# Optimization experiments

Measured on AMD Instinct MI355X. Metric: run time of the kernel, lower is better.

Reference implementation:

```python
import jax, jax.numpy as jnp
import numpy as np

B, T, D, H, E = 4, 2048, 1024, 4096, 8


def setup_inputs() -> dict:
    key = jax.random.key(0)
    ks = jax.random.split(key, 7)
    x = jax.random.normal(ks[0], (B, T, D), dtype=jnp.float32)
    # Gate: Linear(D, E)
    Wg = jax.random.normal(ks[1], (D, E), dtype=jnp.float32) / np.sqrt(D)
    bg = jax.random.normal(ks[2], (E,), dtype=jnp.float32) * 0.01
    # Experts: E x [Linear(D,H), ReLU, Linear(H,D)] (dropout inactive at eval)
    W1 = jax.random.normal(ks[3], (E, D, H), dtype=jnp.float32) / np.sqrt(D)
    b1 = jax.random.normal(ks[4], (E, H), dtype=jnp.float32) * 0.01
    W2 = jax.random.normal(ks[5], (E, H, D), dtype=jnp.float32) / np.sqrt(H)
    b2 = jax.random.normal(ks[6], (E, D), dtype=jnp.float32) * 0.01
    return {"x": x, "Wg": Wg, "bg": bg, "W1": W1, "b1": b1, "W2": W2, "b2": b2}


def reference(x, Wg, bg, W1, b1, W2, b2):
    # Gate + hard top-1 routing
    gate_scores = x @ Wg + bg                      # [B,T,E]
    top1 = jnp.argmax(gate_scores, axis=-1)        # [B,T]
    onehot = jax.nn.one_hot(top1, Wg.shape[-1], dtype=x.dtype)  # [B,T,E]
    # Dense: every expert MLP over all tokens (matches original's masked
    # formulation: x*mask == x on selected tokens, output re-masked).
    h = jax.nn.relu(jnp.einsum('btd,edh->beth', x, W1) + b1[None, :, None, :])
    y = jnp.einsum('beth,ehd->betd', h, W2) + b2[None, :, None, :]
    # Masked combine: keep only the token's chosen expert output
    out = jnp.einsum('betd,bte->btd', y, onehot)
    return out
```

## Files before the change

### kernel.cpp

```cpp
#include <hip/hip_runtime.h>
#include <hip/hip_bf16.h>
#include <stdint.h>

#define NTOK 8192
#define DDIM 1024
#define HDIM 4096
#define NEXP 8
#define MAXWL 72

typedef __attribute__((ext_vector_type(4))) float f32x4;
typedef __attribute__((ext_vector_type(8))) short s16x8;
typedef __attribute__((ext_vector_type(8))) unsigned short u16x8;

__device__ __forceinline__ unsigned short f2bf(float f) {
  union { float f; unsigned int u; } v; v.f = f;
  unsigned int u = v.u;
  u += 0x7FFFu + ((u >> 16) & 1u);
  return (unsigned short)(u >> 16);
}

typedef __attribute__((address_space(3))) unsigned char lds_u8;
typedef const __attribute__((address_space(1))) unsigned char glb_u8;

__device__ __forceinline__ void load_lds16(const void* g, void* l) {
  __builtin_amdgcn_global_load_lds((glb_u8*)g, (lds_u8*)l, 16, 0, 0);
}

__global__ __launch_bounds__(256) void gate_kernel(
    const float* __restrict__ x, const float* __restrict__ Wg,
    const float* __restrict__ bg, int* __restrict__ counts,
    int* __restrict__ lists) {
  const int lane = threadIdx.x & 63;
  const int tok = blockIdx.x * 4 + (threadIdx.x >> 6);
  const float* xr = x + (size_t)tok * DDIM;
  double acc[NEXP];
#pragma unroll
  for (int e = 0; e < NEXP; ++e) acc[e] = 0.0;
#pragma unroll 4
  for (int it = 0; it < DDIM / 64; ++it) {
    const int d = it * 64 + lane;
    const float xv = xr[d];
    const f32x4 w0 = *(const f32x4*)(Wg + (size_t)d * NEXP);
    const f32x4 w1 = *(const f32x4*)(Wg + (size_t)d * NEXP + 4);
#pragma unroll
    for (int j = 0; j < 4; ++j) {
      acc[j]     += (double)xv * (double)w0[j];
      acc[4 + j] += (double)xv * (double)w1[j];
    }
  }
#pragma unroll
  for (int e = 0; e < NEXP; ++e) {
    double v = acc[e];
#pragma unroll
    for (int off = 32; off > 0; off >>= 1) v += __shfl_xor(v, off, 64);
    acc[e] = v;
  }
  if (lane == 0) {
    int best = 0;
    double bv = acc[0] + (double)bg[0];
#pragma unroll
    for (int e = 1; e < NEXP; ++e) {
      const double v = acc[e] + (double)bg[e];
      if (v > bv) { bv = v; best = e; }
    }
    const int pos = atomicAdd(&counts[best], 1);
    lists[best * NTOK + pos] = tok;
  }
}

__global__ void offs_kernel(const int* __restrict__ counts, int* __restrict__ offs,
                            int* __restrict__ wl) {
  int s = 0;
#pragma unroll
  for (int e = 0; e < NEXP; ++e) { offs[e] = s; s += counts[e]; }
  offs[NEXP] = s;
  int n = 0;
  for (int e = 0; e < NEXP; ++e) {
    const int nb = (counts[e] + 127) >> 7;
    for (int b = 0; b < nb; ++b) wl[n++] = (e << 20) | b;
  }
  offs[NEXP + 1] = n;
}

__global__ __launch_bounds__(256) void gather_conv_kernel(
    const float* __restrict__ x, const int* __restrict__ offs,
    const int* __restrict__ lists, int* __restrict__ stok,
    unsigned short* __restrict__ xbs) {
  const int p = blockIdx.x * 4 + (threadIdx.x >> 6);
  const int lane = threadIdx.x & 63;
  int e = 0;
#pragma unroll
  for (int k = 1; k < NEXP; ++k) e += (p >= offs[k]) ? 1 : 0;
  const int tok = lists[e * NTOK + (p - offs[e])];
  if (lane == 0) stok[p] = tok;
  const float* src = x + (size_t)tok * DDIM + lane * 16;
  unsigned short* dst = xbs + (size_t)p * DDIM + lane * 16;
#pragma unroll
  for (int q = 0; q < 2; ++q) {
    const f32x4 a = *(const f32x4*)(src + q * 8);
    const f32x4 b = *(const f32x4*)(src + q * 8 + 4);
    u16x8 o;
#pragma unroll
    for (int j = 0; j < 4; ++j) { o[j] = f2bf(a[j]); o[4 + j] = f2bf(b[j]); }
    *(u16x8*)(dst + q * 8) = o;
  }
}

__global__ __launch_bounds__(256) void transpose_conv_kernel(
    const float* __restrict__ in, unsigned short* __restrict__ out,
    int R, int C) {
  __shared__ unsigned short T[64][66];
  const int e = blockIdx.z;
  const float* ine = in + (size_t)e * R * C;
  unsigned short* oute = out + (size_t)e * C * R;
  const int c0 = blockIdx.x * 64, r0 = blockIdx.y * 64;
  const int t = threadIdx.x;
  const int tr = t >> 4, tc4 = (t & 15) * 4;
#pragma unroll
  for (int p = 0; p < 4; ++p) {
    const int r = tr + p * 16;
    const f32x4 v = *(const f32x4*)(ine + (size_t)(r0 + r) * C + c0 + tc4);
#pragma unroll
    for (int j = 0; j < 4; ++j) T[r][tc4 + j] = f2bf(v[j]);
  }
  __syncthreads();
#pragma unroll
  for (int p = 0; p < 4; ++p) {
    const int c = tr + p * 16;
    ushort4 o;
    o.x = T[tc4 + 0][c]; o.y = T[tc4 + 1][c];
    o.z = T[tc4 + 2][c]; o.w = T[tc4 + 3][c];
    *(ushort4*)(oute + (size_t)(c0 + c) * R + r0 + tc4) = o;
  }
}

template <int K, int N, bool FUSE1>
__global__ __launch_bounds__(256, 2) void ffn_kernel(
    const unsigned short* __restrict__ A, const unsigned short* __restrict__ Bt,
    const float* __restrict__ bias, const int* __restrict__ counts,
    const int* __restrict__ offs, const int* __restrict__ wl,
    const int* __restrict__ stok, unsigned short* __restrict__ outb,
    float* __restrict__ outf) {
  constexpr int BM = 128, BN = 128;
  constexpr int MF = 4, NF = 4;
  constexpr int NT = K / 64;
  static_assert((NT & 1) == 0 && NT >= 4, "");

  if ((int)blockIdx.y >= offs[NEXP + 1]) return;
  const int wle = wl[blockIdx.y];
  const int e = wle >> 20;
  const int bx = wle & 0xFFFFF;
  const int cnt = counts[e];
  const int row0 = offs[e] + bx * BM;
  const int col0 = blockIdx.x * BN;

  __shared__ __align__(16) unsigned short As0[BM][64];
  __shared__ __align__(16) unsigned short Bs0[BN][64];
  __shared__ __align__(16) unsigned short As1[BM][64];
  __shared__ __align__(16) unsigned short Bs1[BN][64];

  const int tid = threadIdx.x;
  const int lane = tid & 63;
  const int w = tid >> 6;
  const int wm = w >> 1;
  const int wn = w & 1;
  const int fr = lane & 15;
  const int fj = lane >> 4;

  const int swz = ((tid & 7) ^ ((tid >> 3) & 7)) * 8;
  const int rb = tid >> 3;
  const unsigned short* srcA[4];
#pragma unroll
  for (int i = 0; i < 4; ++i) {
    int gr = row0 + i * 32 + rb;
    if (gr > NTOK - 1) gr = NTOK - 1;
    srcA[i] = A + (size_t)gr * K + swz;
  }
  const unsigned short* Bte = Bt + (size_t)e * N * K;
  const unsigned short* srcB[4];
#pragma unroll
  for (int i = 0; i < 4; ++i)
    srcB[i] = Bte + (size_t)(col0 + i * 32 + rb) * K + swz;

  f32x4 acc[MF][NF];
#pragma unroll
  for (int m = 0; m < MF; ++m)
#pragma unroll
    for (int n = 0; n < NF; ++n) acc[m][n] = f32x4{0.f, 0.f, 0.f, 0.f};

  auto stage = [&](unsigned short* dA, unsigned short* dB, int k0) {
#pragma unroll
    for (int i = 0; i < 4; ++i)
      load_lds16(srcA[i] + k0, dA + i * 32 * 64 + tid * 8);
#pragma unroll
    for (int i = 0; i < 4; ++i)
      load_lds16(srcB[i] + k0, dB + i * 32 * 64 + tid * 8);
  };

  auto phase = [&](const unsigned short* pA, const unsigned short* pB,
                   unsigned short* nA, unsigned short* nB, int knext,
                   bool do_stage) {
    asm volatile("s_waitcnt vmcnt(0)" ::: "memory");
    __builtin_amdgcn_s_barrier();
    s16x8 af[2][MF], bf[2][NF];
#pragma unroll
    for (int kk = 0; kk < 2; ++kk) {
      const int js = (((kk << 2) + fj) ^ (fr & 7)) << 3;
#pragma unroll
      for (int m = 0; m < MF; ++m)
        af[kk][m] = *(const s16x8*)(pA + (wm * 64 + m * 16 + fr) * 64 + js);
#pragma unroll
      for (int n = 0; n < NF; ++n)
        bf[kk][n] = *(const s16x8*)(pB + (wn * 64 + n * 16 + fr) * 64 + js);
    }
    if (do_stage) stage(nA, nB, knext);
    __builtin_amdgcn_s_setprio(1);
#pragma unroll
    for (int kk = 0; kk < 2; ++kk)
#pragma unroll
      for (int m = 0; m < MF; ++m)
#pragma unroll
        for (int n = 0; n < NF; ++n)
          acc[m][n] = __builtin_amdgcn_mfma_f32_16x16x32_bf16(
              af[kk][m], bf[kk][n], acc[m][n], 0, 0, 0);
    __builtin_amdgcn_s_setprio(0);
  };

  unsigned short* A0 = &As0[0][0];
  unsigned short* B0 = &Bs0[0][0];
  unsigned short* A1 = &As1[0][0];
  unsigned short* B1 = &Bs1[0][0];

  stage(A0, B0, 0);
#pragma unroll 1
  for (int t = 0; t + 2 < NT; t += 2) {
    phase(A0, B0, A1, B1, (t + 1) * 64, true);
    phase(A1, B1, A0, B0, (t + 2) * 64, true);
  }
  phase(A0, B0, A1, B1, (NT - 1) * 64, true);
  phase(A1, B1, A0, B0, 0, false);

#pragma unroll
  for (int n = 0; n < NF; ++n) {
    const int col = col0 + wn * 64 + n * 16 + fr;
    const float bv = bias[e * N + col];
#pragma unroll
    for (int m = 0; m < MF; ++m) {
#pragma unroll
      for (int j = 0; j < 4; ++j) {
        const int rl = wm * 64 + m * 16 + fj * 4 + j;
        if (bx * BM + rl < cnt) {
          if constexpr (FUSE1) {
            outb[(size_t)(row0 + rl) * N + col] = f2bf(fmaxf(acc[m][n][j] + bv, 0.f));
          } else {
            outf[(size_t)stok[row0 + rl] * N + col] = acc[m][n][j] + bv;
          }
        }
      }
    }
  }
}

extern "C" void kernel_launch(void* const* d_in, const int* in_sizes, int n_in,
                              void* d_out, int out_size, void* d_ws, size_t ws_size,
                              hipStream_t stream) {
  (void)in_sizes; (void)n_in; (void)out_size;
  const float* x  = (const float*)d_in[0];
  const float* Wg = (const float*)d_in[1];
  const float* bg = (const float*)d_in[2];
  const float* W1 = (const float*)d_in[3];
  const float* b1 = (const float*)d_in[4];
  const float* W2 = (const float*)d_in[5];
  const float* b2 = (const float*)d_in[6];
  float* out = (float*)d_out;

  char* ws = (char*)d_ws;
  const size_t OFF_CNT = 0;
  const size_t OFF_OFF = 128;
  const size_t OFF_WL  = 256;
  const size_t OFF_LST = 1024;
  const size_t OFF_STK = OFF_LST + (size_t)NEXP * NTOK * 4;
  const size_t OFF_XBS = OFF_STK + (size_t)NTOK * 4;
  const size_t OFF_HS  = OFF_XBS + (size_t)NTOK * DDIM * 2;
  const size_t OFF_WT  = OFF_HS + (size_t)NTOK * HDIM * 2;
  const size_t NEED    = OFF_WT + (size_t)NEXP * DDIM * HDIM * 2;
  if (ws_size < NEED) return;

  int* counts = (int*)(ws + OFF_CNT);
  int* offs   = (int*)(ws + OFF_OFF);
  int* wl     = (int*)(ws + OFF_WL);
  int* lists  = (int*)(ws + OFF_LST);
  int* stok   = (int*)(ws + OFF_STK);
  unsigned short* xbs = (unsigned short*)(ws + OFF_XBS);
  unsigned short* Hs  = (unsigned short*)(ws + OFF_HS);
  unsigned short* Wt  = (unsigned short*)(ws + OFF_WT);

  hipMemsetAsync(counts, 0, 128, stream);
  gate_kernel<<<NTOK / 4, 256, 0, stream>>>(x, Wg, bg, counts, lists);
  offs_kernel<<<1, 1, 0, stream>>>(counts, offs, wl);
  gather_conv_kernel<<<NTOK / 4, 256, 0, stream>>>(x, offs, lists, stok, xbs);

  transpose_conv_kernel<<<dim3(HDIM / 64, DDIM / 64, NEXP), 256, 0, stream>>>(
      W1, Wt, DDIM, HDIM);
  ffn_kernel<DDIM, HDIM, true>
      <<<dim3(HDIM / 128, MAXWL), 256, 0, stream>>>(
          xbs, Wt, b1, counts, offs, wl, stok, Hs, nullptr);
  transpose_conv_kernel<<<dim3(DDIM / 64, HDIM / 64, NEXP), 256, 0, stream>>>(
      W2, Wt, HDIM, DDIM);
  ffn_kernel<HDIM, DDIM, false>
      <<<dim3(DDIM / 128, MAXWL), 256, 0, stream>>>(
          Hs, Wt, b2, counts, offs, wl, stok, nullptr, out);
}
```

Measured before the change: 502.4 us.

## Use 256x256 tiles with 4-stage LDS pipeline and XCD-aware block remap

The grouped expert GEMMs move from 128x128 tiles with 256 threads and a double-buffered BK=64 loop to 256x256 tiles with 512 threads and a 4-stage BK=32 ring of global_load_lds buffers, using partial vmcnt waits so loads stay in flight. The worklist now uses 256-row blocks (MAXWL reduced to 48), and a 1D grid is remapped so consecutive logical tiles land on the same XCD for L2 reuse. The aim is to raise arithmetic intensity per LDS byte, hide memory latency more deeply, and improve cache locality. The cost is more padding waste per expert, higher register pressure from 32 accumulators per wave, and fewer workgroups for load balance.

```diff
diff --git a/kernel.cpp b/kernel.cpp
--- a/kernel.cpp
+++ b/kernel.cpp
@@ -6,7 +6,7 @@
 #define DDIM 1024
 #define HDIM 4096
 #define NEXP 8
-#define MAXWL 72
+#define MAXWL 48
 
 typedef __attribute__((ext_vector_type(4))) float f32x4;
 typedef __attribute__((ext_vector_type(8))) short s16x8;
@@ -24,6 +24,12 @@
 
 __device__ __forceinline__ void load_lds16(const void* g, void* l) {
   __builtin_amdgcn_global_load_lds((glb_u8*)g, (lds_u8*)l, 16, 0, 0);
+}
+
+template <int VM> __device__ __forceinline__ void wait_vm() {
+  if constexpr (VM == 8) asm volatile("s_waitcnt vmcnt(8)" ::: "memory");
+  else if constexpr (VM == 4) asm volatile("s_waitcnt vmcnt(4)" ::: "memory");
+  else asm volatile("s_waitcnt vmcnt(0)" ::: "memory");
 }
 
 __global__ __launch_bounds__(256) void gate_kernel(
@@ -76,7 +82,7 @@
   offs[NEXP] = s;
   int n = 0;
   for (int e = 0; e < NEXP; ++e) {
-    const int nb = (counts[e] + 127) >> 7;
+    const int nb = (counts[e] + 255) >> 8;
     for (int b = 0; b < nb; ++b) wl[n++] = (e << 20) | b;
   }
   offs[NEXP + 1] = n;
@@ -134,122 +140,115 @@
   }
 }
 
-template <int K, int N, bool FUSE1>
-__global__ __launch_bounds__(256, 2) void ffn_kernel(
+template <int K, int N, int NCB, bool FUSE1>
+__global__ __launch_bounds__(512, 2) void ffn_kernel(
     const unsigned short* __restrict__ A, const unsigned short* __restrict__ Bt,
     const float* __restrict__ bias, const int* __restrict__ counts,
     const int* __restrict__ offs, const int* __restrict__ wl,
     const int* __restrict__ stok, unsigned short* __restrict__ outb,
     float* __restrict__ outf) {
-  constexpr int BM = 128, BN = 128;
-  constexpr int MF = 4, NF = 4;
-  constexpr int NT = K / 64;
-  static_assert((NT & 1) == 0 && NT >= 4, "");
-
-  if ((int)blockIdx.y >= offs[NEXP + 1]) return;
-  const int wle = wl[blockIdx.y];
+  constexpr int NT = K / 32;
+  static_assert((NT & 3) == 0 && NT >= 8, "");
+  constexpr int NWG = NCB * MAXWL;
+  static_assert((NWG & 7) == 0, "");
+
+  const int d = blockIdx.x;
+  const int logical = (d & 7) * (NWG / 8) + (d >> 3);
+  const int col0 = (logical / MAXWL) * 256;
+  const int wli = logical % MAXWL;
+  if (wli >= offs[NEXP + 1]) return;
+  const int wle = wl[wli];
   const int e = wle >> 20;
   const int bx = wle & 0xFFFFF;
   const int cnt = counts[e];
-  const int row0 = offs[e] + bx * BM;
-  const int col0 = blockIdx.x * BN;
-
-  __shared__ __align__(16) unsigned short As0[BM][64];
-  __shared__ __align__(16) unsigned short Bs0[BN][64];
-  __shared__ __align__(16) unsigned short As1[BM][64];
-  __shared__ __align__(16) unsigned short Bs1[BN][64];
+  const int row0 = offs[e] + bx * 256;
+
+  __shared__ __align__(16) unsigned short As0[256 * 32], Bs0[256 * 32];
+  __shared__ __align__(16) unsigned short As1[256 * 32], Bs1[256 * 32];
+  __shared__ __align__(16) unsigned short As2[256 * 32], Bs2[256 * 32];
+  __shared__ __align__(16) unsigned short As3[256 * 32], Bs3[256 * 32];
 
   const int tid = threadIdx.x;
   const int lane = tid & 63;
   const int w = tid >> 6;
-  const int wm = w >> 1;
-  const int wn = w & 1;
+  const int wm = w >> 2;
+  const int wn = w & 3;
   const int fr = lane & 15;
   const int fj = lane >> 4;
 
-  const int swz = ((tid & 7) ^ ((tid >> 3) & 7)) * 8;
-  const int rb = tid >> 3;
-  const unsigned short* srcA[4];
-#pragma unroll
-  for (int i = 0; i < 4; ++i) {
-    int gr = row0 + i * 32 + rb;
-    if (gr > NTOK - 1) gr = NTOK - 1;
-    srcA[i] = A + (size_t)gr * K + swz;
-  }
+  const int swsrc = (((tid & 3) ^ ((tid >> 2) & 3) ^ ((tid >> 4) & 3))) * 8;
+  int gr0 = row0 + (tid >> 2);        if (gr0 > NTOK - 1) gr0 = NTOK - 1;
+  int gr1 = row0 + 128 + (tid >> 2);  if (gr1 > NTOK - 1) gr1 = NTOK - 1;
+  const unsigned short* srcA0 = A + (size_t)gr0 * K + swsrc;
+  const unsigned short* srcA1 = A + (size_t)gr1 * K + swsrc;
   const unsigned short* Bte = Bt + (size_t)e * N * K;
-  const unsigned short* srcB[4];
-#pragma unroll
-  for (int i = 0; i < 4; ++i)
-    srcB[i] = Bte + (size_t)(col0 + i * 32 + rb) * K + swz;
-
-  f32x4 acc[MF][NF];
-#pragma unroll
-  for (int m = 0; m < MF; ++m)
-#pragma unroll
-    for (int n = 0; n < NF; ++n) acc[m][n] = f32x4{0.f, 0.f, 0.f, 0.f};
-
-  auto stage = [&](unsigned short* dA, unsigned short* dB, int k0) {
-#pragma unroll
-    for (int i = 0; i < 4; ++i)
-      load_lds16(srcA[i] + k0, dA + i * 32 * 64 + tid * 8);
-#pragma unroll
-    for (int i = 0; i < 4; ++i)
-      load_lds16(srcB[i] + k0, dB + i * 32 * 64 + tid * 8);
+  const unsigned short* srcB0 = Bte + (size_t)(col0 + (tid >> 2)) * K + swsrc;
+  const unsigned short* srcB1 = Bte + (size_t)(col0 + 128 + (tid >> 2)) * K + swsrc;
+
+  const int js = ((fj ^ (fr & 3) ^ ((fr >> 2) & 3))) * 8;
+
+  f32x4 acc[8][4];
+#pragma unroll
+  for (int m = 0; m < 8; ++m)
+#pragma unroll
+    for (int n = 0; n < 4; ++n) acc[m][n] = f32x4{0.f, 0.f, 0.f, 0.f};
+
+  auto stage = [&](unsigned short* nA, unsigned short* nB, int kel) {
+    load_lds16(srcA0 + kel, nA + tid * 8);
+    load_lds16(srcA1 + kel, nA + 4096 + tid * 8);
+    load_lds16(srcB0 + kel, nB + tid * 8);
+    load_lds16(srcB1 + kel, nB + 4096 + tid * 8);
   };
 
-  auto phase = [&](const unsigned short* pA, const unsigned short* pB,
-                   unsigned short* nA, unsigned short* nB, int knext,
-                   bool do_stage) {
-    asm volatile("s_waitcnt vmcnt(0)" ::: "memory");
+  auto body = [&](const unsigned short* pA, const unsigned short* pB,
+                  unsigned short* nA, unsigned short* nB, int knext,
+                  bool do_stage) {
     __builtin_amdgcn_s_barrier();
-    s16x8 af[2][MF], bf[2][NF];
-#pragma unroll
-    for (int kk = 0; kk < 2; ++kk) {
-      const int js = (((kk << 2) + fj) ^ (fr & 7)) << 3;
-#pragma unroll
-      for (int m = 0; m < MF; ++m)
-        af[kk][m] = *(const s16x8*)(pA + (wm * 64 + m * 16 + fr) * 64 + js);
-#pragma unroll
-      for (int n = 0; n < NF; ++n)
-        bf[kk][n] = *(const s16x8*)(pB + (wn * 64 + n * 16 + fr) * 64 + js);
-    }
+    asm volatile("" ::: "memory");
     if (do_stage) stage(nA, nB, knext);
+    s16x8 af[8], bf[4];
+#pragma unroll
+    for (int m = 0; m < 8; ++m)
+      af[m] = *(const s16x8*)(pA + (wm * 128 + m * 16 + fr) * 32 + js);
+#pragma unroll
+    for (int n = 0; n < 4; ++n)
+      bf[n] = *(const s16x8*)(pB + (wn * 64 + n * 16 + fr) * 32 + js);
     __builtin_amdgcn_s_setprio(1);
 #pragma unroll
-    for (int kk = 0; kk < 2; ++kk)
-#pragma unroll
-      for (int m = 0; m < MF; ++m)
-#pragma unroll
-        for (int n = 0; n < NF; ++n)
-          acc[m][n] = __builtin_amdgcn_mfma_f32_16x16x32_bf16(
-              af[kk][m], bf[kk][n], acc[m][n], 0, 0, 0);
+    for (int m = 0; m < 8; ++m)
+#pragma unroll
+      for (int n = 0; n < 4; ++n)
+        acc[m][n] = __builtin_amdgcn_mfma_f32_16x16x32_bf16(af[m], bf[n],
+                                                            acc[m][n], 0, 0, 0);
     __builtin_amdgcn_s_setprio(0);
   };
 
-  unsigned short* A0 = &As0[0][0];
-  unsigned short* B0 = &Bs0[0][0];
-  unsigned short* A1 = &As1[0][0];
-  unsigned short* B1 = &Bs1[0][0];
-
-  stage(A0, B0, 0);
+  stage(As0, Bs0, 0);
+  stage(As1, Bs1, 32);
+  stage(As2, Bs2, 64);
+
 #pragma unroll 1
-  for (int t = 0; t + 2 < NT; t += 2) {
-    phase(A0, B0, A1, B1, (t + 1) * 64, true);
-    phase(A1, B1, A0, B0, (t + 2) * 64, true);
-  }
-  phase(A0, B0, A1, B1, (NT - 1) * 64, true);
-  phase(A1, B1, A0, B0, 0, false);
-
-#pragma unroll
-  for (int n = 0; n < NF; ++n) {
+  for (int t = 0; t < NT - 4; t += 4) {
+    wait_vm<8>(); body(As0, Bs0, As3, Bs3, (t + 3) * 32, true);
+    wait_vm<8>(); body(As1, Bs1, As0, Bs0, (t + 4) * 32, true);
+    wait_vm<8>(); body(As2, Bs2, As1, Bs1, (t + 5) * 32, true);
+    wait_vm<8>(); body(As3, Bs3, As2, Bs2, (t + 6) * 32, true);
+  }
+  wait_vm<8>(); body(As0, Bs0, As3, Bs3, (NT - 1) * 32, true);
+  wait_vm<8>(); body(As1, Bs1, nullptr, nullptr, 0, false);
+  wait_vm<4>(); body(As2, Bs2, nullptr, nullptr, 0, false);
+  wait_vm<0>(); body(As3, Bs3, nullptr, nullptr, 0, false);
+
+#pragma unroll
+  for (int n = 0; n < 4; ++n) {
     const int col = col0 + wn * 64 + n * 16 + fr;
     const float bv = bias[e * N + col];
 #pragma unroll
-    for (int m = 0; m < MF; ++m) {
+    for (int m = 0; m < 8; ++m) {
 #pragma unroll
       for (int j = 0; j < 4; ++j) {
-        const int rl = wm * 64 + m * 16 + fj * 4 + j;
-        if (bx * BM + rl < cnt) {
+        const int rl = wm * 128 + m * 16 + fj * 4 + j;
+        if (bx * 256 + rl < cnt) {
           if constexpr (FUSE1) {
             outb[(size_t)(row0 + rl) * N + col] = f2bf(fmaxf(acc[m][n][j] + bv, 0.f));
           } else {
@@ -302,12 +301,12 @@
 
   transpose_conv_kernel<<<dim3(HDIM / 64, DDIM / 64, NEXP), 256, 0, stream>>>(
       W1, Wt, DDIM, HDIM);
-  ffn_kernel<DDIM, HDIM, true>
-      <<<dim3(HDIM / 128, MAXWL), 256, 0, stream>>>(
+  ffn_kernel<DDIM, HDIM, HDIM / 256, true>
+      <<<dim3((HDIM / 256) * MAXWL), 512, 0, stream>>>(
           xbs, Wt, b1, counts, offs, wl, stok, Hs, nullptr);
   transpose_conv_kernel<<<dim3(DDIM / 64, HDIM / 64, NEXP), 256, 0, stream>>>(
       W2, Wt, HDIM, DDIM);
-  ffn_kernel<HDIM, DDIM, false>
-      <<<dim3(DDIM / 128, MAXWL), 256, 0, stream>>>(
+  ffn_kernel<HDIM, DDIM, DDIM / 256, false>
+      <<<dim3((DDIM / 256) * MAXWL), 512, 0, stream>>>(
           Hs, Wt, b2, counts, offs, wl, stok, nullptr, out);
 }
```

Result: faster. 469.7 us (-6.5%).

## Enlarge FFN GEMM tiles, remap workgroups per XCD, widen transpose stores

Applied to the files above, without the earlier changes.

The expert FFN GEMM is templated on tile and wave shape. It now uses 256x256 tiles with 8 waves for the first GEMM and 256x128 for the second, and the work list is rebuilt in 256-row chunks. The grid becomes 1D with an XCD-aware remap of the block index. The K-loop is restructured so the next stage is issued before compute, with fragment loads split per k-substep. The weight transpose also writes 8-element vectors instead of 4. Larger tiles raise data reuse and cut redundant weight loads, at the cost of more padded rows per expert, fewer workgroups and higher register and LDS pressure.

```diff
diff --git a/kernel.cpp b/kernel.cpp
--- a/kernel.cpp
+++ b/kernel.cpp
@@ -6,7 +6,7 @@
 #define DDIM 1024
 #define HDIM 4096
 #define NEXP 8
-#define MAXWL 72
+#define MAXWL 48
 
 typedef __attribute__((ext_vector_type(4))) float f32x4;
 typedef __attribute__((ext_vector_type(8))) short s16x8;
@@ -76,7 +76,7 @@
   offs[NEXP] = s;
   int n = 0;
   for (int e = 0; e < NEXP; ++e) {
-    const int nb = (counts[e] + 127) >> 7;
+    const int nb = (counts[e] + 255) >> 8;
     for (int b = 0; b < nb; ++b) wl[n++] = (e << 20) | b;
   }
   offs[NEXP + 1] = n;
@@ -124,63 +124,69 @@
     for (int j = 0; j < 4; ++j) T[r][tc4 + j] = f2bf(v[j]);
   }
   __syncthreads();
-#pragma unroll
-  for (int p = 0; p < 4; ++p) {
-    const int c = tr + p * 16;
-    ushort4 o;
-    o.x = T[tc4 + 0][c]; o.y = T[tc4 + 1][c];
-    o.z = T[tc4 + 2][c]; o.w = T[tc4 + 3][c];
-    *(ushort4*)(oute + (size_t)(c0 + c) * R + r0 + tc4) = o;
-  }
-}
-
-template <int K, int N, bool FUSE1>
-__global__ __launch_bounds__(256, 2) void ffn_kernel(
+  const int cc = t >> 3, rr8 = (t & 7) * 8;
+#pragma unroll
+  for (int p = 0; p < 2; ++p) {
+    const int c = cc + p * 32;
+    u16x8 o;
+#pragma unroll
+    for (int j = 0; j < 8; ++j) o[j] = T[rr8 + j][c];
+    *(u16x8*)(oute + (size_t)(c0 + c) * R + r0 + rr8) = o;
+  }
+}
+
+template <int BM, int BN, int WM, int WN, int K, int N, bool FUSE1>
+__global__ __launch_bounds__(64 * WM * WN, 2) void ffn_kernel(
     const unsigned short* __restrict__ A, const unsigned short* __restrict__ Bt,
     const float* __restrict__ bias, const int* __restrict__ counts,
     const int* __restrict__ offs, const int* __restrict__ wl,
     const int* __restrict__ stok, unsigned short* __restrict__ outb,
     float* __restrict__ outf) {
-  constexpr int BM = 128, BN = 128;
-  constexpr int MF = 4, NF = 4;
+  constexpr int MF = BM / (WM * 16);
+  constexpr int NF = BN / (WN * 16);
+  constexpr int ISS_A = BM / 64;
+  constexpr int ISS_B = BN / 64;
   constexpr int NT = K / 64;
-  static_assert((NT & 1) == 0 && NT >= 4, "");
-
-  if ((int)blockIdx.y >= offs[NEXP + 1]) return;
-  const int wle = wl[blockIdx.y];
+  constexpr int NCB = N / BN;
+  constexpr int NWG = NCB * MAXWL;
+  static_assert((NWG & 7) == 0 && (NT & 1) == 0 && NT >= 4, "");
+
+  const int d = blockIdx.x;
+  const int logical = (d & 7) * (NWG / 8) + (d >> 3);
+  const int col0 = (logical / MAXWL) * BN;
+  const int wli = logical % MAXWL;
+  if (wli >= offs[NEXP + 1]) return;
+  const int wle = wl[wli];
   const int e = wle >> 20;
   const int bx = wle & 0xFFFFF;
   const int cnt = counts[e];
   const int row0 = offs[e] + bx * BM;
-  const int col0 = blockIdx.x * BN;
-
-  __shared__ __align__(16) unsigned short As0[BM][64];
-  __shared__ __align__(16) unsigned short Bs0[BN][64];
-  __shared__ __align__(16) unsigned short As1[BM][64];
-  __shared__ __align__(16) unsigned short Bs1[BN][64];
+
+  __shared__ __align__(16) unsigned short As0[BM * 64], Bs0[BN * 64];
+  __shared__ __align__(16) unsigned short As1[BM * 64], Bs1[BN * 64];
 
   const int tid = threadIdx.x;
   const int lane = tid & 63;
   const int w = tid >> 6;
-  const int wm = w >> 1;
-  const int wn = w & 1;
+  const int wm = w / WN;
+  const int wn = w % WN;
   const int fr = lane & 15;
   const int fj = lane >> 4;
 
   const int swz = ((tid & 7) ^ ((tid >> 3) & 7)) * 8;
   const int rb = tid >> 3;
-  const unsigned short* srcA[4];
-#pragma unroll
-  for (int i = 0; i < 4; ++i) {
-    int gr = row0 + i * 32 + rb;
+  const unsigned short* srcA[ISS_A];
+#pragma unroll
+  for (int i = 0; i < ISS_A; ++i) {
+    int gr = row0 + i * 64 + rb;
     if (gr > NTOK - 1) gr = NTOK - 1;
     srcA[i] = A + (size_t)gr * K + swz;
   }
   const unsigned short* Bte = Bt + (size_t)e * N * K;
-  const unsigned short* srcB[4];
-#pragma unroll
-  for (int i = 0; i < 4; ++i)
-    srcB[i] = Bte + (size_t)(col0 + i * 32 + rb) * K + swz;
+  const unsigned short* srcB[ISS_B];
+#pragma unroll
+  for (int i = 0; i < ISS_B; ++i)
+    srcB[i] = Bte + (size_t)(col0 + i * 64 + rb) * K + swz;
 
   f32x4 acc[MF][NF];
 #pragma unroll
@@ -190,65 +196,65 @@
 
   auto stage = [&](unsigned short* dA, unsigned short* dB, int k0) {
 #pragma unroll
-    for (int i = 0; i < 4; ++i)
-      load_lds16(srcA[i] + k0, dA + i * 32 * 64 + tid * 8);
-#pragma unroll
-    for (int i = 0; i < 4; ++i)
-      load_lds16(srcB[i] + k0, dB + i * 32 * 64 + tid * 8);
+    for (int i = 0; i < ISS_A; ++i)
+      load_lds16(srcA[i] + k0, dA + i * 64 * 64 + tid * 8);
+#pragma unroll
+    for (int i = 0; i < ISS_B; ++i)
+      load_lds16(srcB[i] + k0, dB + i * 64 * 64 + tid * 8);
   };
 
-  auto phase = [&](const unsigned short* pA, const unsigned short* pB,
-                   unsigned short* nA, unsigned short* nB, int knext,
-                   bool do_stage) {
+  auto compute = [&](const unsigned short* pA, const unsigned short* pB) {
+#pragma unroll
+    for (int kk = 0; kk < 2; ++kk) {
+      const int js = (((kk << 2) + fj) ^ (fr & 7)) << 3;
+      s16x8 af[MF], bf[NF];
+#pragma unroll
+      for (int m = 0; m < MF; ++m)
+        af[m] = *(const s16x8*)(pA + (wm * MF * 16 + m * 16 + fr) * 64 + js);
+#pragma unroll
+      for (int n = 0; n < NF; ++n)
+        bf[n] = *(const s16x8*)(pB + (wn * NF * 16 + n * 16 + fr) * 64 + js);
+      __builtin_amdgcn_s_setprio(1);
+#pragma unroll
+      for (int m = 0; m < MF; ++m)
+#pragma unroll
+        for (int n = 0; n < NF; ++n)
+          acc[m][n] = __builtin_amdgcn_mfma_f32_16x16x32_bf16(af[m], bf[n],
+                                                              acc[m][n], 0, 0, 0);
+      __builtin_amdgcn_s_setprio(0);
+    }
+  };
+
+  stage(As0, Bs0, 0);
+  asm volatile("s_waitcnt vmcnt(0)" ::: "memory");
+  __builtin_amdgcn_s_barrier();
+
+#pragma unroll 1
+  for (int t = 0; t < NT - 2; t += 2) {
+    stage(As1, Bs1, (t + 1) * 64);
+    compute(As0, Bs0);
     asm volatile("s_waitcnt vmcnt(0)" ::: "memory");
     __builtin_amdgcn_s_barrier();
-    s16x8 af[2][MF], bf[2][NF];
-#pragma unroll
-    for (int kk = 0; kk < 2; ++kk) {
-      const int js = (((kk << 2) + fj) ^ (fr & 7)) << 3;
-#pragma unroll
-      for (int m = 0; m < MF; ++m)
-        af[kk][m] = *(const s16x8*)(pA + (wm * 64 + m * 16 + fr) * 64 + js);
-#pragma unroll
-      for (int n = 0; n < NF; ++n)
-        bf[kk][n] = *(const s16x8*)(pB + (wn * 64 + n * 16 + fr) * 64 + js);
-    }
-    if (do_stage) stage(nA, nB, knext);
-    __builtin_amdgcn_s_setprio(1);
-#pragma unroll
-    for (int kk = 0; kk < 2; ++kk)
-#pragma unroll
-      for (int m = 0; m < MF; ++m)
-#pragma unroll
-        for (int n = 0; n < NF; ++n)
-          acc[m][n] = __builtin_amdgcn_mfma_f32_16x16x32_bf16(
-              af[kk][m], bf[kk][n], acc[m][n], 0, 0, 0);
-    __builtin_amdgcn_s_setprio(0);
-  };
-
-  unsigned short* A0 = &As0[0][0];
-  unsigned short* B0 = &Bs0[0][0];
-  unsigned short* A1 = &As1[0][0];
-  unsigned short* B1 = &Bs1[0][0];
-
-  stage(A0, B0, 0);
-#pragma unroll 1
-  for (int t = 0; t + 2 < NT; t += 2) {
-    phase(A0, B0, A1, B1, (t + 1) * 64, true);
-    phase(A1, B1, A0, B0, (t + 2) * 64, true);
-  }
-  phase(A0, B0, A1, B1, (NT - 1) * 64, true);
-  phase(A1, B1, A0, B0, 0, false);
+    stage(As0, Bs0, (t + 2) * 64);
+    compute(As1, Bs1);
+    asm volatile("s_waitcnt vmcnt(0)" ::: "memory");
+    __builtin_amdgcn_s_barrier();
+  }
+  stage(As1, Bs1, (NT - 1) * 64);
+  compute(As0, Bs0);
+  asm volatile("s_waitcnt vmcnt(0)" ::: "memory");
+  __builtin_amdgcn_s_barrier();
+  compute(As1, Bs1);
 
 #pragma unroll
   for (int n = 0; n < NF; ++n) {
-    const int col = col0 + wn * 64 + n * 16 + fr;
+    const int col = col0 + wn * NF * 16 + n * 16 + fr;
     const float bv = bias[e * N + col];
 #pragma unroll
     for (int m = 0; m < MF; ++m) {
 #pragma unroll
       for (int j = 0; j < 4; ++j) {
-        const int rl = wm * 64 + m * 16 + fj * 4 + j;
+        const int rl = wm * MF * 16 + m * 16 + fj * 4 + j;
         if (bx * BM + rl < cnt) {
           if constexpr (FUSE1) {
             outb[(size_t)(row0 + rl) * N + col] = f2bf(fmaxf(acc[m][n][j] + bv, 0.f));
@@ -302,12 +308,12 @@
 
   transpose_conv_kernel<<<dim3(HDIM / 64, DDIM / 64, NEXP), 256, 0, stream>>>(
       W1, Wt, DDIM, HDIM);
-  ffn_kernel<DDIM, HDIM, true>
-      <<<dim3(HDIM / 128, MAXWL), 256, 0, stream>>>(
+  ffn_kernel<256, 256, 2, 4, DDIM, HDIM, true>
+      <<<dim3((HDIM / 256) * MAXWL), 512, 0, stream>>>(
           xbs, Wt, b1, counts, offs, wl, stok, Hs, nullptr);
   transpose_conv_kernel<<<dim3(DDIM / 64, HDIM / 64, NEXP), 256, 0, stream>>>(
       W2, Wt, HDIM, DDIM);
-  ffn_kernel<HDIM, DDIM, false>
-      <<<dim3(DDIM / 128, MAXWL), 256, 0, stream>>>(
+  ffn_kernel<256, 128, 4, 2, HDIM, DDIM, false>
+      <<<dim3((DDIM / 128) * MAXWL), 512, 0, stream>>>(
           Hs, Wt, b2, counts, offs, wl, stok, nullptr, out);
 }
```

New measurement: 509.9 us. About the same (+1.5%).
